# Optimization experiments

Hardware: AMD Instinct MI355X
Metric: run time of the kernel (lower is better)

## Reference

```python
import jax, jax.numpy as jnp
import numpy as np

B = 4            # batch size (max batch index + 1, fixed by construction)
H, W = 176, 200  # feature_map_size; x in [0,H), y in [0,W)
C_IN, C_OUT = 128, 256
BW, N = 4096, 64
EPS = 1e-5       # torch LayerNorm default


def setup_inputs() -> dict:
    key = jax.random.key(0)
    k1, k2, k3, k4, k5, k6, k7 = jax.random.split(key, 7)
    window_features = jax.random.normal(k1, (BW, N, C_IN), jnp.float32)
    bidx = jax.random.randint(k2, (BW, N, 1), 0, B)
    xidx = jax.random.randint(k3, (BW, N, 1), -8, H + 8)   # includes invalid coords
    yidx = jax.random.randint(k4, (BW, N, 1), -8, W + 8)
    window_indices = jnp.concatenate([bidx, xidx, yidx], axis=-1).astype(jnp.int32)
    norm_weight = 1.0 + 0.1 * jax.random.normal(k5, (C_IN,), jnp.float32)
    norm_bias = 0.1 * jax.random.normal(k6, (C_IN,), jnp.float32)
    lin_weight = jax.random.normal(k7, (C_OUT, C_IN), jnp.float32) / np.sqrt(C_IN)
    return {"window_features": window_features, "window_indices": window_indices,
            "norm_weight": norm_weight, "norm_bias": norm_bias, "lin_weight": lin_weight}


def reference(window_features, window_indices, norm_weight, norm_bias, lin_weight):
    # window_features: (BW, N, C_IN); window_indices: (BW, N, 3) = (batch, x, y)
    bw, n, c = window_features.shape
    feats = window_features.reshape(-1, c)                # (P, C)
    idx = window_indices.reshape(-1, 3)
    b, x, y = idx[:, 0], idx[:, 1], idx[:, 2]
    valid = (x >= 0) & (x < H) & (y >= 0) & (y < W)

    # unique + index_add_ + sparse-to-dense == scatter-add into dense BEV grid.
    # Invalid rows are routed out-of-bounds and dropped.
    bs = jnp.where(valid, b, B)
    xs = jnp.where(valid, x, 0)
    ys = jnp.where(valid, y, 0)
    # dense layout matches spconv: spatial_shape=[W, H], indices (b, y, x)
    dense_sum = jnp.zeros((B, W, H, c), window_features.dtype)
    dense_sum = dense_sum.at[bs, ys, xs].add(feats, mode="drop")
    count = jnp.zeros((B, W, H), window_features.dtype)
    count = count.at[bs, ys, xs].add(1.0, mode="drop")
    occupied = count > 0                                   # cells holding a unique voxel

    # LayerNorm over C (patch_norm=True) then Linear (bias=False) on occupied cells
    mu = jnp.mean(dense_sum, axis=-1, keepdims=True)
    var = jnp.mean(jnp.square(dense_sum - mu), axis=-1, keepdims=True)
    normed = (dense_sum - mu) * jax.lax.rsqrt(var + EPS) * norm_weight + norm_bias
    dense_out = jnp.einsum("bwhc,oc->bwho", normed, lin_weight)
    dense_out = jnp.where(occupied[..., None], dense_out, 0.0)  # empty cells stay zero

    # gather_operation: pull dense features back to each valid window point
    gathered = dense_out[jnp.where(valid, b, 0), ys, xs]   # (P, C_OUT)
    new_feats = jnp.where(valid[:, None], gathered, 0.0).reshape(bw, n, C_OUT)
    return new_feats, window_indices
```

## Files before the change

### kernel.cpp

```cpp
#include <hip/hip_runtime.h>
#include <stdint.h>

#define HH 176
#define WW 200
#define BB 4
#define CIN 128
#define COUT 256
#define NPTS (4096 * 64)
#define CELLS (BB * WW * HH)
#define FEAT_OUT_ELEMS ((size_t)NPTS * COUT)
#define CAP 32
#define TCELLS 32
#define LDSWF 132
#define LDSW16 260
#define FLATCAP 1024

typedef __attribute__((ext_vector_type(8))) short bf16x8;
typedef __attribute__((ext_vector_type(4))) float f32x4;

__device__ __forceinline__ unsigned short f2bf(float f) {
    union { float f; unsigned int u; } c; c.f = f;
    unsigned int u = c.u;
    u += 0x7fffu + ((u >> 16) & 1u);
    return (unsigned short)(u >> 16);
}
__device__ __forceinline__ float bf2f(unsigned int h16) {
    union { unsigned int u; float f; } c; c.u = h16 << 16;
    return c.f;
}

__global__ __launch_bounds__(256) void prep_kernel(
    const float* __restrict__ lw, unsigned short* __restrict__ wb,
    int* __restrict__ counts)
{
    int i = blockIdx.x * 256 + threadIdx.x;
    if (i < COUT * CIN) wb[i] = f2bf(lw[i]);
    counts[i] = 0;
}

__global__ __launch_bounds__(256) void build_kernel(
    const int* __restrict__ idx, int* __restrict__ counts, int* __restrict__ plist,
    float* __restrict__ out_idx, float* __restrict__ out_feats)
{
    __shared__ unsigned char validf[256];
    int tid = threadIdx.x;
    int p0 = blockIdx.x * 256;
    int p = p0 + tid;
    int b = idx[3 * p], x = idx[3 * p + 1], y = idx[3 * p + 2];
    out_idx[3 * p]     = (float)b;
    out_idx[3 * p + 1] = (float)x;
    out_idx[3 * p + 2] = (float)y;
    bool valid = ((unsigned)x < HH && (unsigned)y < WW);
    validf[tid] = valid ? 1 : 0;
    if (valid) {
        int cell = (b * WW + y) * HH + x;
        int slot = atomicAdd(&counts[cell], 1);
        if (slot < CAP) plist[(size_t)cell * CAP + slot] = p;
    }
    __syncthreads();
    int w = tid >> 6, lane = tid & 63;
    float4 z = { 0.0f, 0.0f, 0.0f, 0.0f };
    for (int v = w; v < 256; v += 4)
        if (!validf[v])
            *(float4*)(out_feats + (size_t)(p0 + v) * COUT + lane * 4) = z;
}

__global__ __launch_bounds__(256) void fused_kernel(
    const float* __restrict__ feats,
    const unsigned short* __restrict__ Wb,
    const int* __restrict__ counts,
    const int* __restrict__ plist,
    const float* __restrict__ nw, const float* __restrict__ nb,
    float* __restrict__ out)
{
    __shared__ float accf[TCELLS * LDSWF];
    __shared__ unsigned short normedl[TCELLS * LDSWF];
    __shared__ int fpid[FLATCAP];
    __shared__ unsigned char fcell[FLATCAP];
    __shared__ int scnt[TCELLS];
    __shared__ int nflat;
    unsigned short* out16 = (unsigned short*)accf;

    int tid = threadIdx.x;
    int w = tid >> 6, lane = tid & 63;
    int l15 = lane & 15, g = lane >> 4;
    int kgrp = g * 8, orow = g * 4;
    int c0 = blockIdx.x * TCELLS;

    if (tid == 0) nflat = 0;
    if (tid < TCELLS) {
        int cnt = counts[c0 + tid];
        scnt[tid] = cnt < CAP ? cnt : CAP;
    }
    for (int i = tid; i < TCELLS * LDSWF; i += 256) accf[i] = 0.0f;
    __syncthreads();

    if (tid < TCELLS) {
        int cnt = scnt[tid];
        if (cnt > 0) {
            int base = atomicAdd(&nflat, cnt);
            for (int s = 0; s < cnt; ++s) {
                fpid[base + s] = plist[(size_t)(c0 + tid) * CAP + s];
                fcell[base + s] = (unsigned char)tid;
            }
        }
    }
    __syncthreads();
    int nt = nflat;

    {
        int k = w;
        float2 v0 = {0.0f, 0.0f};
        int cc0 = 0;
        if (k < nt) {
            int pid = fpid[k]; cc0 = fcell[k];
            v0 = *(const float2*)(feats + (size_t)pid * CIN + lane * 2);
        }
        while (k < nt) {
            int kn = k + 4;
            float2 v1 = {0.0f, 0.0f};
            int cc1 = 0;
            if (kn < nt) {
                int pid = fpid[kn]; cc1 = fcell[kn];
                v1 = *(const float2*)(feats + (size_t)pid * CIN + lane * 2);
            }
            atomicAdd(&accf[cc0 * LDSWF + lane * 2], v0.x);
            atomicAdd(&accf[cc0 * LDSWF + lane * 2 + 1], v0.y);
            k = kn; cc0 = cc1; v0 = v1;
        }
    }

    bf16x8 a[4][4];
    #pragma unroll
    for (int i = 0; i < 4; ++i)
        #pragma unroll
        for (int kk = 0; kk < 4; ++kk)
            a[i][kk] = *(const bf16x8*)(Wb + (size_t)(((w * 4 + i) * 16 + l15) * CIN) + kgrp + kk * 32);

    float w0 = nw[lane * 2], w1 = nw[lane * 2 + 1];
    float b0 = nb[lane * 2], b1 = nb[lane * 2 + 1];

    __syncthreads();

    for (int c = w; c < TCELLS; c += 4) {
        float a0 = accf[c * LDSWF + lane * 2];
        float a1 = accf[c * LDSWF + lane * 2 + 1];
        float s = a0 + a1;
        float ss = a0 * a0 + a1 * a1;
        #pragma unroll
        for (int m = 32; m >= 1; m >>= 1) {
            s  += __shfl_xor(s, m, 64);
            ss += __shfl_xor(ss, m, 64);
        }
        float mu  = s * (1.0f / 128.0f);
        float var = ss * (1.0f / 128.0f) - mu * mu;
        float inv = rsqrtf(var + 1e-5f);
        ushort2 st;
        st.x = f2bf((a0 - mu) * inv * w0 + b0);
        st.y = f2bf((a1 - mu) * inv * w1 + b1);
        *(ushort2*)(&normedl[c * LDSWF + lane * 2]) = st;
    }
    __syncthreads();

    #pragma unroll
    for (int tj = 0; tj < 2; ++tj) {
        bf16x8 bb[4];
        #pragma unroll
        for (int kk = 0; kk < 4; ++kk)
            bb[kk] = *(const bf16x8*)(normedl + (tj * 16 + l15) * LDSWF + kgrp + kk * 32);
        f32x4 acc[4];
        #pragma unroll
        for (int i = 0; i < 4; ++i) acc[i] = (f32x4){0.0f, 0.0f, 0.0f, 0.0f};
        #pragma unroll
        for (int kk = 0; kk < 4; ++kk)
            #pragma unroll
            for (int i = 0; i < 4; ++i)
                acc[i] = __builtin_amdgcn_mfma_f32_16x16x32_bf16(a[i][kk], bb[kk], acc[i], 0, 0, 0);
        #pragma unroll
        for (int i = 0; i < 4; ++i) {
            int o = w * 64 + i * 16 + orow;
            ushort4 st;
            st.x = f2bf(acc[i][0]);
            st.y = f2bf(acc[i][1]);
            st.z = f2bf(acc[i][2]);
            st.w = f2bf(acc[i][3]);
            *(ushort4*)(&out16[(tj * 16 + l15) * LDSW16 + o]) = st;
        }
    }
    __syncthreads();

    for (int k = w; k < nt; k += 4) {
        int pid = fpid[k];
        int c = fcell[k];
        ushort4 v = *(const ushort4*)(&out16[c * LDSW16 + lane * 4]);
        float4 o4;
        o4.x = bf2f(v.x);
        o4.y = bf2f(v.y);
        o4.z = bf2f(v.z);
        o4.w = bf2f(v.w);
        *(float4*)(out + (size_t)pid * COUT + lane * 4) = o4;
    }
}

extern "C" void kernel_launch(void* const* d_in, const int* in_sizes, int n_in,
                              void* d_out, int out_size, void* d_ws, size_t ws_size,
                              hipStream_t stream)
{
    const float* feats = (const float*)d_in[0];
    const int*   idx   = (const int*)d_in[1];
    const float* nw    = (const float*)d_in[2];
    const float* nb    = (const float*)d_in[3];
    const float* lw    = (const float*)d_in[4];
    float* out = (float*)d_out;

    char* ws = (char*)d_ws;
    int* counts = (int*)ws;
    int* plist  = (int*)(ws + (1u << 20));
    unsigned short* wb     = (unsigned short*)(ws + (20u << 20));

    prep_kernel<<<CELLS / 256, 256, 0, stream>>>(lw, wb, counts);
    build_kernel<<<NPTS / 256, 256, 0, stream>>>(idx, counts, plist, out + FEAT_OUT_ELEMS, out);
    fused_kernel<<<CELLS / TCELLS, 256, 0, stream>>>(feats, wb, counts, plist, nw, nb, out);
}
```

Measured before the change: 540.6 us.

## Accumulate cell sums in registers and build point list via wave prefix scan

Replaces the LDS atomic scatter-add of point features with per-wave register accumulation: each wave walks its cells' point lists directly, sums the features and applies LayerNorm without a shared float accumulator. The flat point list is now built with a wave-level prefix scan over counts and packs pid and cell into a single int, in place of an LDS atomic counter and separate arrays. Weight fragments are loaded from global memory inside the MFMA loop rather than preloaded into registers. The intent is to cut LDS atomics, zero-init work, barriers and register/LDS pressure. The cost is more serialized gather latency per wave and repeated weight loads from cache.

```diff
diff --git a/kernel.cpp b/kernel.cpp
--- a/kernel.cpp
+++ b/kernel.cpp
@@ -11,9 +11,10 @@
 #define FEAT_OUT_ELEMS ((size_t)NPTS * COUT)
 #define CAP 32
 #define TCELLS 32
-#define LDSWF 132
-#define LDSW16 260
-#define FLATCAP 1024
+#define LDSWN 132
+#define LDSWO 260
+#define FLATCAP 512
+#define PIDMASK 0x3FFFF
 
 typedef __attribute__((ext_vector_type(8))) short bf16x8;
 typedef __attribute__((ext_vector_type(4))) float f32x4;
@@ -73,13 +74,10 @@
     const float* __restrict__ nw, const float* __restrict__ nb,
     float* __restrict__ out)
 {
-    __shared__ float accf[TCELLS * LDSWF];
-    __shared__ unsigned short normedl[TCELLS * LDSWF];
-    __shared__ int fpid[FLATCAP];
-    __shared__ unsigned char fcell[FLATCAP];
+    __shared__ unsigned short normedl[TCELLS * LDSWN];
+    __shared__ unsigned short out16[TCELLS * LDSWO];
+    __shared__ int fpl[FLATCAP];
     __shared__ int scnt[TCELLS];
-    __shared__ int nflat;
-    unsigned short* out16 = (unsigned short*)accf;
 
     int tid = threadIdx.x;
     int w = tid >> 6, lane = tid & 63;
@@ -87,95 +85,113 @@
     int kgrp = g * 8, orow = g * 4;
     int c0 = blockIdx.x * TCELLS;
 
-    if (tid == 0) nflat = 0;
-    if (tid < TCELLS) {
-        int cnt = counts[c0 + tid];
-        scnt[tid] = cnt < CAP ? cnt : CAP;
-    }
-    for (int i = tid; i < TCELLS * LDSWF; i += 256) accf[i] = 0.0f;
-    __syncthreads();
-
-    if (tid < TCELLS) {
-        int cnt = scnt[tid];
-        if (cnt > 0) {
-            int base = atomicAdd(&nflat, cnt);
-            for (int s = 0; s < cnt; ++s) {
-                fpid[base + s] = plist[(size_t)(c0 + tid) * CAP + s];
-                fcell[base + s] = (unsigned char)tid;
-            }
-        }
-    }
-    __syncthreads();
-    int nt = nflat;
-
-    {
-        int k = w;
-        float2 v0 = {0.0f, 0.0f};
-        int cc0 = 0;
-        if (k < nt) {
-            int pid = fpid[k]; cc0 = fcell[k];
-            v0 = *(const float2*)(feats + (size_t)pid * CIN + lane * 2);
-        }
-        while (k < nt) {
-            int kn = k + 4;
-            float2 v1 = {0.0f, 0.0f};
-            int cc1 = 0;
-            if (kn < nt) {
-                int pid = fpid[kn]; cc1 = fcell[kn];
-                v1 = *(const float2*)(feats + (size_t)pid * CIN + lane * 2);
-            }
-            atomicAdd(&accf[cc0 * LDSWF + lane * 2], v0.x);
-            atomicAdd(&accf[cc0 * LDSWF + lane * 2 + 1], v0.y);
-            k = kn; cc0 = cc1; v0 = v1;
-        }
-    }
-
-    bf16x8 a[4][4];
-    #pragma unroll
-    for (int i = 0; i < 4; ++i)
-        #pragma unroll
-        for (int kk = 0; kk < 4; ++kk)
-            a[i][kk] = *(const bf16x8*)(Wb + (size_t)(((w * 4 + i) * 16 + l15) * CIN) + kgrp + kk * 32);
-
+    if (tid < 8) {
+        int4 c4 = *(const int4*)(counts + c0 + tid * 4);
+        scnt[tid * 4 + 0] = c4.x < CAP ? c4.x : CAP;
+        scnt[tid * 4 + 1] = c4.y < CAP ? c4.y : CAP;
+        scnt[tid * 4 + 2] = c4.z < CAP ? c4.z : CAP;
+        scnt[tid * 4 + 3] = c4.w < CAP ? c4.w : CAP;
+    }
     float w0 = nw[lane * 2], w1 = nw[lane * 2 + 1];
     float b0 = nb[lane * 2], b1 = nb[lane * 2 + 1];
-
-    __syncthreads();
-
-    for (int c = w; c < TCELLS; c += 4) {
-        float a0 = accf[c * LDSWF + lane * 2];
-        float a1 = accf[c * LDSWF + lane * 2 + 1];
-        float s = a0 + a1;
-        float ss = a0 * a0 + a1 * a1;
-        #pragma unroll
-        for (int m = 32; m >= 1; m >>= 1) {
-            s  += __shfl_xor(s, m, 64);
-            ss += __shfl_xor(ss, m, 64);
-        }
-        float mu  = s * (1.0f / 128.0f);
-        float var = ss * (1.0f / 128.0f) - mu * mu;
-        float inv = rsqrtf(var + 1e-5f);
-        ushort2 st;
-        st.x = f2bf((a0 - mu) * inv * w0 + b0);
-        st.y = f2bf((a1 - mu) * inv * w1 + b1);
-        *(ushort2*)(&normedl[c * LDSWF + lane * 2]) = st;
+    __syncthreads();
+
+    int l31 = lane & 31;
+    int cs = scnt[l31];
+    int v = cs;
+    #pragma unroll
+    for (int off = 1; off < 32; off <<= 1) {
+        int t = __shfl_up(v, off, 64);
+        if (l31 >= off) v += t;
+    }
+    int nt = __shfl(v, 31, 64);
+    if (nt > FLATCAP) nt = FLATCAP;
+    int myexcl = v - cs;
+
+    if (tid < 64) {
+        int cell = l31;
+        int cnt = cs;
+        int base = myexcl;
+        int tag = cell << 18;
+        if (lane < 32) {
+            int4 p4 = *(const int4*)(plist + (size_t)(c0 + cell) * CAP);
+            if (cnt > 0 && base + 0 < FLATCAP) fpl[base + 0] = (p4.x & PIDMASK) | tag;
+            if (cnt > 1 && base + 1 < FLATCAP) fpl[base + 1] = (p4.y & PIDMASK) | tag;
+            if (cnt > 2 && base + 2 < FLATCAP) fpl[base + 2] = (p4.z & PIDMASK) | tag;
+            if (cnt > 3 && base + 3 < FLATCAP) fpl[base + 3] = (p4.w & PIDMASK) | tag;
+        } else if (cnt > 4) {
+            int4 p4 = *(const int4*)(plist + (size_t)(c0 + cell) * CAP + 4);
+            if (base + 4 < FLATCAP)            fpl[base + 4] = (p4.x & PIDMASK) | tag;
+            if (cnt > 5 && base + 5 < FLATCAP) fpl[base + 5] = (p4.y & PIDMASK) | tag;
+            if (cnt > 6 && base + 6 < FLATCAP) fpl[base + 6] = (p4.z & PIDMASK) | tag;
+            if (cnt > 7 && base + 7 < FLATCAP) fpl[base + 7] = (p4.w & PIDMASK) | tag;
+            for (int s = 8; s < cnt; ++s) {
+                int pp = plist[(size_t)(c0 + cell) * CAP + s];
+                if (base + s < FLATCAP) fpl[base + s] = (pp & PIDMASK) | tag;
+            }
+        }
+    }
+
+    #pragma unroll
+    for (int grp = 0; grp < 2; ++grp) {
+        int4 pq[4];
+        #pragma unroll
+        for (int ci = 0; ci < 4; ++ci) {
+            int c = w + (grp * 4 + ci) * 4;
+            pq[ci] = *(const int4*)(plist + (size_t)(c0 + c) * CAP);
+        }
+        #pragma unroll
+        for (int ci = 0; ci < 4; ++ci) {
+            int c = w + (grp * 4 + ci) * 4;
+            int cnt = scnt[c];
+            float s0 = 0.0f, s1 = 0.0f;
+            if (cnt > 0) { float2 t = *(const float2*)(feats + (size_t)(pq[ci].x) * CIN + lane * 2); s0 += t.x; s1 += t.y; }
+            if (cnt > 1) { float2 t = *(const float2*)(feats + (size_t)(pq[ci].y) * CIN + lane * 2); s0 += t.x; s1 += t.y; }
+            if (cnt > 2) { float2 t = *(const float2*)(feats + (size_t)(pq[ci].z) * CIN + lane * 2); s0 += t.x; s1 += t.y; }
+            if (cnt > 3) { float2 t = *(const float2*)(feats + (size_t)(pq[ci].w) * CIN + lane * 2); s0 += t.x; s1 += t.y; }
+            if (cnt > 4) {
+                int4 q2 = *(const int4*)(plist + (size_t)(c0 + c) * CAP + 4);
+                { float2 t = *(const float2*)(feats + (size_t)(q2.x) * CIN + lane * 2); s0 += t.x; s1 += t.y; }
+                if (cnt > 5) { float2 t = *(const float2*)(feats + (size_t)(q2.y) * CIN + lane * 2); s0 += t.x; s1 += t.y; }
+                if (cnt > 6) { float2 t = *(const float2*)(feats + (size_t)(q2.z) * CIN + lane * 2); s0 += t.x; s1 += t.y; }
+                if (cnt > 7) { float2 t = *(const float2*)(feats + (size_t)(q2.w) * CIN + lane * 2); s0 += t.x; s1 += t.y; }
+                for (int s = 8; s < cnt; ++s) {
+                    int pid = plist[(size_t)(c0 + c) * CAP + s];
+                    float2 t = *(const float2*)(feats + (size_t)pid * CIN + lane * 2);
+                    s0 += t.x; s1 += t.y;
+                }
+            }
+            float s = s0 + s1, ss = s0 * s0 + s1 * s1;
+            #pragma unroll
+            for (int m = 32; m >= 1; m >>= 1) {
+                s  += __shfl_xor(s, m, 64);
+                ss += __shfl_xor(ss, m, 64);
+            }
+            float mu  = s * (1.0f / 128.0f);
+            float var = ss * (1.0f / 128.0f) - mu * mu;
+            float inv = rsqrtf(var + 1e-5f);
+            ushort2 st;
+            st.x = f2bf((s0 - mu) * inv * w0 + b0);
+            st.y = f2bf((s1 - mu) * inv * w1 + b1);
+            *(ushort2*)(&normedl[c * LDSWN + lane * 2]) = st;
+        }
     }
     __syncthreads();
 
     #pragma unroll
     for (int tj = 0; tj < 2; ++tj) {
-        bf16x8 bb[4];
-        #pragma unroll
-        for (int kk = 0; kk < 4; ++kk)
-            bb[kk] = *(const bf16x8*)(normedl + (tj * 16 + l15) * LDSWF + kgrp + kk * 32);
         f32x4 acc[4];
         #pragma unroll
         for (int i = 0; i < 4; ++i) acc[i] = (f32x4){0.0f, 0.0f, 0.0f, 0.0f};
         #pragma unroll
-        for (int kk = 0; kk < 4; ++kk)
+        for (int kk = 0; kk < 4; ++kk) {
+            bf16x8 bbv = *(const bf16x8*)(&normedl[(tj * 16 + l15) * LDSWN + kgrp + kk * 32]);
             #pragma unroll
-            for (int i = 0; i < 4; ++i)
-                acc[i] = __builtin_amdgcn_mfma_f32_16x16x32_bf16(a[i][kk], bb[kk], acc[i], 0, 0, 0);
+            for (int i = 0; i < 4; ++i) {
+                bf16x8 av = *(const bf16x8*)(Wb + (size_t)(((w * 4 + i) * 16 + l15) * CIN) + kgrp + kk * 32);
+                acc[i] = __builtin_amdgcn_mfma_f32_16x16x32_bf16(av, bbv, acc[i], 0, 0, 0);
+            }
+        }
         #pragma unroll
         for (int i = 0; i < 4; ++i) {
             int o = w * 64 + i * 16 + orow;
@@ -184,20 +200,21 @@
             st.y = f2bf(acc[i][1]);
             st.z = f2bf(acc[i][2]);
             st.w = f2bf(acc[i][3]);
-            *(ushort4*)(&out16[(tj * 16 + l15) * LDSW16 + o]) = st;
+            *(ushort4*)(&out16[(tj * 16 + l15) * LDSWO + o]) = st;
         }
     }
     __syncthreads();
 
     for (int k = w; k < nt; k += 4) {
-        int pid = fpid[k];
-        int c = fcell[k];
-        ushort4 v = *(const ushort4*)(&out16[c * LDSW16 + lane * 4]);
+        int vpk = fpl[k];
+        int pid = vpk & PIDMASK;
+        int c = vpk >> 18;
+        ushort4 vv = *(const ushort4*)(&out16[c * LDSWO + lane * 4]);
         float4 o4;
-        o4.x = bf2f(v.x);
-        o4.y = bf2f(v.y);
-        o4.z = bf2f(v.z);
-        o4.w = bf2f(v.w);
+        o4.x = bf2f(vv.x);
+        o4.y = bf2f(vv.y);
+        o4.z = bf2f(vv.z);
+        o4.w = bf2f(vv.w);
         *(float4*)(out + (size_t)pid * COUT + lane * 4) = o4;
     }
 }
```

New measurement: 473.0 us. 1.14x faster.

## Make fused kernel wave-independent with register accumulation and per-wave GEMM

Applied to the files above, without the earlier changes.

Each wave now owns 16 cells and does its own gather, LayerNorm, MFMA projection and scatter, so block-wide barriers, LDS atomics and the shared flat point list go away. Features are summed in registers, with the first four point ids per cell prefetched as an int4. Each wave runs the full 256-column GEMM against its 16 cells, streaming weights from global/L2 instead of keeping a per-wave weight slice in registers. This trades more weight traffic per wave for less synchronisation and less LDS contention.

```diff
diff --git a/kernel.cpp b/kernel.cpp
--- a/kernel.cpp
+++ b/kernel.cpp
@@ -10,10 +10,9 @@
 #define CELLS (BB * WW * HH)
 #define FEAT_OUT_ELEMS ((size_t)NPTS * COUT)
 #define CAP 32
-#define TCELLS 32
-#define LDSWF 132
-#define LDSW16 260
-#define FLATCAP 1024
+#define WCELLS 16
+#define LDSWN 136
+#define LDSWO 264
 
 typedef __attribute__((ext_vector_type(8))) short bf16x8;
 typedef __attribute__((ext_vector_type(4))) float f32x4;
@@ -73,80 +72,43 @@
     const float* __restrict__ nw, const float* __restrict__ nb,
     float* __restrict__ out)
 {
-    __shared__ float accf[TCELLS * LDSWF];
-    __shared__ unsigned short normedl[TCELLS * LDSWF];
-    __shared__ int fpid[FLATCAP];
-    __shared__ unsigned char fcell[FLATCAP];
-    __shared__ int scnt[TCELLS];
-    __shared__ int nflat;
-    unsigned short* out16 = (unsigned short*)accf;
+    __shared__ unsigned short stage[4][WCELLS * LDSWO];
 
     int tid = threadIdx.x;
     int w = tid >> 6, lane = tid & 63;
     int l15 = lane & 15, g = lane >> 4;
     int kgrp = g * 8, orow = g * 4;
-    int c0 = blockIdx.x * TCELLS;
-
-    if (tid == 0) nflat = 0;
-    if (tid < TCELLS) {
-        int cnt = counts[c0 + tid];
-        scnt[tid] = cnt < CAP ? cnt : CAP;
-    }
-    for (int i = tid; i < TCELLS * LDSWF; i += 256) accf[i] = 0.0f;
-    __syncthreads();
-
-    if (tid < TCELLS) {
-        int cnt = scnt[tid];
-        if (cnt > 0) {
-            int base = atomicAdd(&nflat, cnt);
-            for (int s = 0; s < cnt; ++s) {
-                fpid[base + s] = plist[(size_t)(c0 + tid) * CAP + s];
-                fcell[base + s] = (unsigned char)tid;
-            }
-        }
-    }
-    __syncthreads();
-    int nt = nflat;
-
-    {
-        int k = w;
-        float2 v0 = {0.0f, 0.0f};
-        int cc0 = 0;
-        if (k < nt) {
-            int pid = fpid[k]; cc0 = fcell[k];
-            v0 = *(const float2*)(feats + (size_t)pid * CIN + lane * 2);
-        }
-        while (k < nt) {
-            int kn = k + 4;
-            float2 v1 = {0.0f, 0.0f};
-            int cc1 = 0;
-            if (kn < nt) {
-                int pid = fpid[kn]; cc1 = fcell[kn];
-                v1 = *(const float2*)(feats + (size_t)pid * CIN + lane * 2);
-            }
-            atomicAdd(&accf[cc0 * LDSWF + lane * 2], v0.x);
-            atomicAdd(&accf[cc0 * LDSWF + lane * 2 + 1], v0.y);
-            k = kn; cc0 = cc1; v0 = v1;
-        }
-    }
-
-    bf16x8 a[4][4];
-    #pragma unroll
-    for (int i = 0; i < 4; ++i)
-        #pragma unroll
-        for (int kk = 0; kk < 4; ++kk)
-            a[i][kk] = *(const bf16x8*)(Wb + (size_t)(((w * 4 + i) * 16 + l15) * CIN) + kgrp + kk * 32);
+    int c0 = blockIdx.x * 64 + w * WCELLS;
+    unsigned short* buf = &stage[w][0];
 
     float w0 = nw[lane * 2], w1 = nw[lane * 2 + 1];
     float b0 = nb[lane * 2], b1 = nb[lane * 2 + 1];
 
-    __syncthreads();
+    int cnts[WCELLS];
+    int4 pq[WCELLS];
+    #pragma unroll
+    for (int c = 0; c < WCELLS; ++c) {
+        int n = counts[c0 + c];
+        cnts[c] = n < CAP ? n : CAP;
+        pq[c] = *(const int4*)(plist + (size_t)(c0 + c) * CAP);
+    }
 
-    for (int c = w; c < TCELLS; c += 4) {
-        float a0 = accf[c * LDSWF + lane * 2];
-        float a1 = accf[c * LDSWF + lane * 2 + 1];
-        float s = a0 + a1;
-        float ss = a0 * a0 + a1 * a1;
+    #pragma unroll
+    for (int c = 0; c < WCELLS; ++c) {
+        int cnt = cnts[c];
+        float s0 = 0.0f, s1 = 0.0f;
+        if (cnt > 0) { float2 t = *(const float2*)(feats + (size_t)pq[c].x * CIN + lane * 2); s0 += t.x; s1 += t.y; }
+        if (cnt > 1) { float2 t = *(const float2*)(feats + (size_t)pq[c].y * CIN + lane * 2); s0 += t.x; s1 += t.y; }
+        if (cnt > 2) { float2 t = *(const float2*)(feats + (size_t)pq[c].z * CIN + lane * 2); s0 += t.x; s1 += t.y; }
+        if (cnt > 3) { float2 t = *(const float2*)(feats + (size_t)pq[c].w * CIN + lane * 2); s0 += t.x; s1 += t.y; }
+        if (cnt > 4) {
+            for (int s = 4; s < cnt; ++s) {
+                int pid = plist[(size_t)(c0 + c) * CAP + s];
+                float2 t = *(const float2*)(feats + (size_t)pid * CIN + lane * 2);
+                s0 += t.x; s1 += t.y;
+            }
+        }
+        float s = s0 + s1, ss = s0 * s0 + s1 * s1;
         #pragma unroll
         for (int m = 32; m >= 1; m >>= 1) {
             s  += __shfl_xor(s, m, 64);
@@ -156,49 +118,53 @@
         float var = ss * (1.0f / 128.0f) - mu * mu;
         float inv = rsqrtf(var + 1e-5f);
         ushort2 st;
-        st.x = f2bf((a0 - mu) * inv * w0 + b0);
-        st.y = f2bf((a1 - mu) * inv * w1 + b1);
-        *(ushort2*)(&normedl[c * LDSWF + lane * 2]) = st;
+        st.x = f2bf((s0 - mu) * inv * w0 + b0);
+        st.y = f2bf((s1 - mu) * inv * w1 + b1);
+        *(ushort2*)(&buf[c * LDSWN + lane * 2]) = st;
     }
-    __syncthreads();
+
+    bf16x8 bfr[4];
+    #pragma unroll
+    for (int kk = 0; kk < 4; ++kk)
+        bfr[kk] = *(const bf16x8*)(&buf[l15 * LDSWN + kgrp + kk * 32]);
 
     #pragma unroll
-    for (int tj = 0; tj < 2; ++tj) {
-        bf16x8 bb[4];
+    for (int i = 0; i < 16; ++i) {
+        f32x4 acc = (f32x4){0.0f, 0.0f, 0.0f, 0.0f};
         #pragma unroll
-        for (int kk = 0; kk < 4; ++kk)
-            bb[kk] = *(const bf16x8*)(normedl + (tj * 16 + l15) * LDSWF + kgrp + kk * 32);
-        f32x4 acc[4];
-        #pragma unroll
-        for (int i = 0; i < 4; ++i) acc[i] = (f32x4){0.0f, 0.0f, 0.0f, 0.0f};
-        #pragma unroll
-        for (int kk = 0; kk < 4; ++kk)
-            #pragma unroll
-            for (int i = 0; i < 4; ++i)
-                acc[i] = __builtin_amdgcn_mfma_f32_16x16x32_bf16(a[i][kk], bb[kk], acc[i], 0, 0, 0);
-        #pragma unroll
-        for (int i = 0; i < 4; ++i) {
-            int o = w * 64 + i * 16 + orow;
-            ushort4 st;
-            st.x = f2bf(acc[i][0]);
-            st.y = f2bf(acc[i][1]);
-            st.z = f2bf(acc[i][2]);
-            st.w = f2bf(acc[i][3]);
-            *(ushort4*)(&out16[(tj * 16 + l15) * LDSW16 + o]) = st;
+        for (int kk = 0; kk < 4; ++kk) {
+            bf16x8 av = *(const bf16x8*)(Wb + (size_t)((i * 16 + l15) * CIN) + kgrp + kk * 32);
+            acc = __builtin_amdgcn_mfma_f32_16x16x32_bf16(av, bfr[kk], acc, 0, 0, 0);
         }
+        ushort4 st;
+        st.x = f2bf(acc[0]);
+        st.y = f2bf(acc[1]);
+        st.z = f2bf(acc[2]);
+        st.w = f2bf(acc[3]);
+        *(ushort4*)(&buf[l15 * LDSWO + i * 16 + orow]) = st;
     }
-    __syncthreads();
 
-    for (int k = w; k < nt; k += 4) {
-        int pid = fpid[k];
-        int c = fcell[k];
-        ushort4 v = *(const ushort4*)(&out16[c * LDSW16 + lane * 4]);
-        float4 o4;
-        o4.x = bf2f(v.x);
-        o4.y = bf2f(v.y);
-        o4.z = bf2f(v.z);
-        o4.w = bf2f(v.w);
-        *(float4*)(out + (size_t)pid * COUT + lane * 4) = o4;
+    #pragma unroll
+    for (int c = 0; c < WCELLS; ++c) {
+        int cnt = cnts[c];
+        if (cnt > 0) {
+            ushort4 v = *(const ushort4*)(&buf[c * LDSWO + lane * 4]);
+            float4 o4;
+            o4.x = bf2f(v.x);
+            o4.y = bf2f(v.y);
+            o4.z = bf2f(v.z);
+            o4.w = bf2f(v.w);
+            *(float4*)(out + (size_t)pq[c].x * COUT + lane * 4) = o4;
+            if (cnt > 1) *(float4*)(out + (size_t)pq[c].y * COUT + lane * 4) = o4;
+            if (cnt > 2) *(float4*)(out + (size_t)pq[c].z * COUT + lane * 4) = o4;
+            if (cnt > 3) *(float4*)(out + (size_t)pq[c].w * COUT + lane * 4) = o4;
+            if (cnt > 4) {
+                for (int s = 4; s < cnt; ++s) {
+                    int pid = plist[(size_t)(c0 + c) * CAP + s];
+                    *(float4*)(out + (size_t)pid * COUT + lane * 4) = o4;
+                }
+            }
+        }
     }
 }
 
@@ -220,5 +186,5 @@
 
     prep_kernel<<<CELLS / 256, 256, 0, stream>>>(lw, wb, counts);
     build_kernel<<<NPTS / 256, 256, 0, stream>>>(idx, counts, plist, out + FEAT_OUT_ELEMS, out);
-    fused_kernel<<<CELLS / TCELLS, 256, 0, stream>>>(feats, wb, counts, plist, nw, nb, out);
+    fused_kernel<<<CELLS / 64, 256, 0, stream>>>(feats, wb, counts, plist, nw, nb, out);
 }
```

Result: faster. 493.9 us (-8.6%).
